# Kernel tuning notes

Hardware: AMD Instinct MI355X
Metric: run time of the kernel (lower is better)

The kernel has to match this reference:

```python
import jax, jax.numpy as jnp
import numpy as np

B, N, D, H = 8, 1024, 768, 4
ALPHA = 0.2      # LeakyReLU negative slope in GraphAttentionLayer
NEG = -9e15      # mask fill value for non-edges (pyGAT convention)


def setup_inputs() -> dict:
    key = jax.random.key(0)
    ks = jax.random.split(key, 8)
    input_emb = jax.random.normal(ks[0], (B, N, D), jnp.float32)
    adj = jax.random.randint(ks[1], (B, N, N), 0, 2, dtype=jnp.int32)
    mask_node = jnp.ones((B, N), jnp.float32)
    s = 1.0 / np.sqrt(D).astype(np.float32)
    W_heads = jax.random.normal(ks[2], (H, D, D), jnp.float32) * s          # per-head W: nfeat->nhid
    a_heads = jax.random.normal(ks[3], (H, 2 * D, 1), jnp.float32) * s      # per-head attention vector a
    W_out = jax.random.normal(ks[4], (H * D, D), jnp.float32) * (1.0 / np.sqrt(H * D).astype(np.float32))
    a_out = jax.random.normal(ks[5], (2 * D, 1), jnp.float32) * s
    w_cls = jax.random.normal(ks[6], (D, 1), jnp.float32) * s               # Classifier.linear1 weight
    b_cls = jnp.zeros((1,), jnp.float32)
    return dict(input_emb=input_emb, adj=adj, mask_node=mask_node,
                W_heads=W_heads, a_heads=a_heads, W_out=W_out, a_out=a_out,
                w_cls=w_cls, b_cls=b_cls)


def _gat_layer(x, adj_mask, W, a, concat):
    # x: [B,N,Fin], W: [Fin,Fout], a: [2*Fout,1], adj_mask: [B,N,N] bool
    Wh = jnp.einsum('bnd,df->bnf', x, W)            # [B,N,Fout]
    Fo = W.shape[1]
    f1 = Wh @ a[:Fo]                                 # [B,N,1] source term
    f2 = Wh @ a[Fo:]                                 # [B,N,1] target term
    e = jax.nn.leaky_relu(f1 + jnp.swapaxes(f2, 1, 2), ALPHA)  # [B,N,N]
    e = jnp.where(adj_mask, e, NEG)
    att = jax.nn.softmax(e, axis=-1)                 # dropout=0 -> no attention dropout
    h = jnp.einsum('bij,bjf->bif', att, Wh)          # [B,N,Fout]
    return jax.nn.elu(h) if concat else h


def reference(input_emb, adj, mask_node, W_heads, a_heads, W_out, a_out, w_cls, b_cls):
    adj_mask = adj > 0
    # multi-head GAT (concat=True heads), vectorized over heads and batch
    heads = jax.vmap(lambda Wi, ai: _gat_layer(input_emb, adj_mask, Wi, ai, True))(W_heads, a_heads)  # [H,B,N,D]
    xx = jnp.moveaxis(heads, 0, 2).reshape(B, N, H * D)  # torch.cat over heads, dim=1 per node
    out = jax.nn.elu(_gat_layer(xx, adj_mask, W_out, a_out, False))
    # dropout_layer(p=0.5) assumed eval mode (identity); residual add
    yy = out + input_emb                               # [B,N,D]
    h = (yy @ w_cls + b_cls)[..., 0]                   # Classifier linear -> [B,N]
    node_scores = jax.nn.sigmoid(h) * mask_node
    return yy, node_scores
```

## Files before the change

### kernel.cpp

```cpp
#include <hip/hip_runtime.h>


typedef unsigned short ushortT;
typedef _Float16 f16;
typedef __attribute__((ext_vector_type(8))) _Float16 f16x8;
typedef __attribute__((ext_vector_type(4))) _Float16 f16x4;
typedef __attribute__((ext_vector_type(4))) float f32x4;
typedef __attribute__((ext_vector_type(2))) float f32x2;
typedef __attribute__((ext_vector_type(8))) unsigned short u16x8;
typedef __attribute__((ext_vector_type(2))) unsigned short u16x2;
typedef __attribute__((ext_vector_type(4))) int i32x4;

#define ALPHA 0.2f

__device__ __forceinline__ float b2f(ushortT u) {
  union { unsigned int i; float f; } c; c.i = ((unsigned int)u) << 16; return c.f;
}
__device__ __forceinline__ ushortT f2b(float f) {
  union { float f; unsigned int u; } c; c.f = f;
  unsigned int u = c.u;
  u += 0x7FFFu + ((u >> 16) & 1u);
  return (ushortT)(u >> 16);
}
__device__ __forceinline__ float* qbuf(char* dout, int flg) {
  return (float*)(dout + (flg ? 25165824L : 12582912L));
}
__device__ __forceinline__ void gld16(const f16* g, f16* l) {
  __builtin_amdgcn_global_load_lds(
      (const __attribute__((address_space(1))) void*)g,
      (__attribute__((address_space(3))) void*)l, 16, 0, 0);
}

__global__ void detect_dtype(const ushortT* __restrict__ X, int* __restrict__ flag,
                             float* __restrict__ Pws, char* __restrict__ dout) {
  __shared__ int s[256];
  int t = threadIdx.x, c = 0;
  for (int i = t; i < 16384; i += 256) {
    int e = (X[2 * i] >> 7) & 0xFF;
    if (e > 140 || e < 100) c++;
  }
  s[t] = c; __syncthreads();
  for (int o = 128; o > 0; o >>= 1) { if (t < o) s[t] += s[t + o]; __syncthreads(); }
  __syncthreads();
  int fl = (s[0] > 1000) ? 1 : 0;
  if (t == 0) *flag = fl;
  float* Qv = qbuf(dout, fl);
#pragma unroll
  for (int i = 0; i < 8; i++) { Pws[t + i * 256] = 0.f; Qv[t + i * 256] = 0.f; }
}

struct GA {
  const void* A; const void* B; void* C; const void* R; const void* avec;
  long aOff, bOff, cOff, rOff, avOff;
  int K, lda, ldb, aRaw, accum, fd, fsel, zmask;
};

template <int MODE, int BSRC>
__device__ void gbody(const GA a, float* Pws, char* dout, int flg,
                      f16* AS, f16* BS) {
  int t = threadIdx.x;
  int n0 = blockIdx.x * 64, m0 = blockIdx.y * 64;
  int aTy = a.aRaw ? (flg ? 2 : 1) : 0;
  float* fv = a.fsel ? qbuf(dout, flg) : Pws;

  if (a.zmask && blockIdx.x == 0 && blockIdx.y == 0) {
    if (a.zmask & 1) {
#pragma unroll
      for (int i = 0; i < 8; i++) Pws[t + i * 256] = 0.f;
    }
    if (a.zmask & 2) {
      float* Qv = qbuf(dout, flg);
#pragma unroll
      for (int i = 0; i < 8; i++) Qv[t + i * 256] = 0.f;
    }
  }

  const f16*     Ah = (const f16*)a.A;
  const ushortT* Au = (const ushortT*)a.A;
  const float*   Af = (const float*)a.A;
  const f16*     Bh = (const f16*)a.B;
  const ushortT* Bu = (const ushortT*)a.B;
  const float*   Bf = (const float*)a.B;

  int lane = t & 63, wid = t >> 6;
  int wr = wid >> 1, wc = wid & 1;
  int lr = lane & 15, lg = lane >> 4, l7 = lane & 7;
  int aRow0 = (wr * 32 + lr) * 64, aRow1 = aRow0 + 16 * 64;
  int bRow0 = (wc * 32 + lr) * 64, bRow1 = bRow0 + 16 * 64;
  int ch0 = ((lg) ^ l7) * 8, ch1 = ((4 + lg) ^ l7) * 8;

  f32x4 acc[2][2];
#pragma unroll
  for (int i = 0; i < 2; i++)
#pragma unroll
    for (int j = 0; j < 2; j++) acc[i][j] = (f32x4){0.f, 0.f, 0.f, 0.f};

  auto compute = [&](int cur) {
    f16* Ac = AS + cur * 4096; f16* Bc = BS + cur * 4096;
#pragma unroll
    for (int kk = 0; kk < 2; kk++) {
      int ch = kk ? ch1 : ch0;
      f16x8 a0 = *(const f16x8*)(Ac + aRow0 + ch);
      f16x8 a1 = *(const f16x8*)(Ac + aRow1 + ch);
      f16x8 b0 = *(const f16x8*)(Bc + bRow0 + ch);
      f16x8 b1 = *(const f16x8*)(Bc + bRow1 + ch);
      acc[0][0] = __builtin_amdgcn_mfma_f32_16x16x32_f16(a0, b0, acc[0][0], 0, 0, 0);
      acc[0][1] = __builtin_amdgcn_mfma_f32_16x16x32_f16(a0, b1, acc[0][1], 0, 0, 0);
      acc[1][0] = __builtin_amdgcn_mfma_f32_16x16x32_f16(a1, b0, acc[1][0], 0, 0, 0);
      acc[1][1] = __builtin_amdgcn_mfma_f32_16x16x32_f16(a1, b1, acc[1][1], 0, 0, 0);
    }
  };

  int KT = a.K >> 6;

  if (BSRC == 0) {
    int gr = lane >> 3, gcn = lane & 7, swz = (gcn ^ (gr & 7)) * 8;
    int isB = wid >> 1, cq4 = (wid & 1) * 4;
    long gA = a.aOff + (long)(m0 + gr) * a.lda + swz;
    long gB = a.bOff + (long)(n0 + gr) * (long)a.K + swz;
    auto stageG = [&](int buf, int kt) {
      if (!isB) {
        const f16* g = Ah + gA + (long)kt * 64;
        f16* dst = AS + buf * 4096;
#pragma unroll
        for (int c = 0; c < 4; c++)
          gld16(g + (long)(cq4 + c) * 8 * a.lda, dst + (cq4 + c) * 512);
      } else {
        const f16* g = Bh + gB + (long)kt * 64;
        f16* dst = BS + buf * 4096;
#pragma unroll
        for (int c = 0; c < 4; c++)
          gld16(g + (long)(cq4 + c) * 8 * a.K, dst + (cq4 + c) * 512);
      }
    };
    stageG(0, 0);
    __syncthreads();
    for (int kt = 0; kt < KT; ++kt) {
      int cur = kt & 1;
      if (kt + 1 < KT) stageG(cur ^ 1, kt + 1);
      compute(cur);
      __syncthreads();
    }
  } else {
    int tq = t >> 2, cq = t & 3;
    long aBase = a.aOff + (long)(m0 + tq) * a.lda + cq * 16;
    int stA0 = tq * 64 + (((2 * cq)     ^ (tq & 7)) * 8);
    int stA1 = tq * 64 + (((2 * cq + 1) ^ (tq & 7)) * 8);
    int q2 = t & 31, cB = t >> 5;
    int nb0 = 2 * q2, nb1 = nb0 + 1;
    int stB0 = nb0 * 64 + ((cB ^ (nb0 & 7)) * 8);
    int stB1 = nb1 * 64 + ((cB ^ (nb1 & 7)) * 8);

    f16x8 ra0, ra1, rb0, rb1;
    auto loadA = [&](int kt) {
      long g = aBase + (long)kt * 64;
      if (aTy == 0) {
        ra0 = *(const f16x8*)(Ah + g);
        ra1 = *(const f16x8*)(Ah + g + 8);
      } else if (aTy == 1) {
        u16x8 v0 = *(const u16x8*)(Au + g);
        u16x8 v1 = *(const u16x8*)(Au + g + 8);
#pragma unroll
        for (int j = 0; j < 8; j++) { ra0[j] = (f16)b2f(v0[j]); ra1[j] = (f16)b2f(v1[j]); }
      } else {
        f32x4 v0 = *(const f32x4*)(Af + g);
        f32x4 v1 = *(const f32x4*)(Af + g + 4);
        f32x4 v2 = *(const f32x4*)(Af + g + 8);
        f32x4 v3 = *(const f32x4*)(Af + g + 12);
#pragma unroll
        for (int j = 0; j < 4; j++) {
          ra0[j] = (f16)v0[j]; ra0[4 + j] = (f16)v1[j];
          ra1[j] = (f16)v2[j]; ra1[4 + j] = (f16)v3[j];
        }
      }
    };
    auto loadB = [&](int kt) {
      long rbase = a.bOff + (long)(kt * 64 + cB * 8) * a.ldb + n0 + 2 * q2;
      if (flg) {
#pragma unroll
        for (int j = 0; j < 8; j++) {
          f32x2 v = *(const f32x2*)(Bf + rbase + (long)j * a.ldb);
          rb0[j] = (f16)v[0]; rb1[j] = (f16)v[1];
        }
      } else {
#pragma unroll
        for (int j = 0; j < 8; j++) {
          u16x2 v = *(const u16x2*)(Bu + rbase + (long)j * a.ldb);
          rb0[j] = (f16)b2f(v[0]); rb1[j] = (f16)b2f(v[1]);
        }
      }
    };
    auto stage = [&](int buf) {
      *(f16x8*)(AS + buf * 4096 + stA0) = ra0;
      *(f16x8*)(AS + buf * 4096 + stA1) = ra1;
      *(f16x8*)(BS + buf * 4096 + stB0) = rb0;
      *(f16x8*)(BS + buf * 4096 + stB1) = rb1;
    };
    loadA(0); loadB(0);
    stage(0);
    loadA(1); loadB(1);
    __syncthreads();
    for (int kt = 0; kt < KT; ++kt) {
      int cur = kt & 1;
      if (kt + 1 < KT) stage(cur ^ 1);
      if (kt + 2 < KT) { loadA(kt + 2); loadB(kt + 2); }
      compute(cur);
      __syncthreads();
    }
  }

  int rowb_base = m0 + wr * 32 + 4 * lg;
  int col_base  = n0 + wc * 32 + lr;

  float a1v[2], a2v[2];
  float p1[2][4], p2[2][4];
  if (a.fd) {
    const float* avf = (const float*)a.avec; const ushortT* avu = (const ushortT*)a.avec;
#pragma unroll
    for (int fn = 0; fn < 2; fn++) {
      int c = n0 + wc * 32 + fn * 16 + lr;
      a1v[fn] = flg ? avf[a.avOff + c]       : b2f(avu[a.avOff + c]);
      a2v[fn] = flg ? avf[a.avOff + 768 + c] : b2f(avu[a.avOff + 768 + c]);
    }
#pragma unroll
    for (int fm = 0; fm < 2; fm++)
#pragma unroll
      for (int r = 0; r < 4; r++) { p1[fm][r] = 0.f; p2[fm][r] = 0.f; }
  }

#pragma unroll
  for (int fm = 0; fm < 2; fm++) {
#pragma unroll
    for (int fn = 0; fn < 2; fn++) {
      int rowb = rowb_base + fm * 16;
      int col  = col_base + fn * 16;
      f32x4 v = acc[fm][fn];
      float fullv[4];
      if (MODE == 4) {
        f16x4 pk;
#pragma unroll
        for (int r = 0; r < 4; r++) { fullv[r] = v[r]; pk[r] = (f16)v[r]; }
        *(f16x4*)((f16*)a.C + (long)col * 1024 + rowb) = pk;
      } else if (MODE == 3) {
        f16* Cc = (f16*)a.C;
        long idx = (long)col * 1024 + rowb;
        f16x4 pk;
        if (a.accum) {
          f16x4 old = *(const f16x4*)(Cc + idx);
#pragma unroll
          for (int r = 0; r < 4; r++) { fullv[r] = (float)old[r] + v[r]; pk[r] = (f16)fullv[r]; }
        } else {
#pragma unroll
          for (int r = 0; r < 4; r++) { fullv[r] = v[r]; pk[r] = (f16)v[r]; }
        }
        *(f16x4*)(Cc + idx) = pk;
      } else {
#pragma unroll
        for (int r = 0; r < 4; r++) {
          int row = rowb + r;
          float x = v[r];
          x = x > 0.f ? x : __expf(x) - 1.f;
          long ci = a.cOff + (long)row * 768 + col;
          if (MODE == 2) {
            long ri = a.rOff + (long)row * 768 + col;
            x += flg ? ((const float*)a.R)[ri] : b2f(((const ushortT*)a.R)[ri]);
            if (flg) ((float*)a.C)[ci] = x;
            else     ((ushortT*)a.C)[ci] = f2b(x);
          } else {
            ((f16*)a.C)[ci] = (f16)x;
          }
        }
      }
      if (a.fd) {
        float ac1 = a1v[fn], ac2 = a2v[fn];
#pragma unroll
        for (int r = 0; r < 4; r++) {
          p1[fm][r] += fullv[r] * ac1;
          p2[fm][r] += fullv[r] * ac2;
        }
      }
    }
  }

  if (a.fd) {
#pragma unroll
    for (int fm = 0; fm < 2; fm++)
#pragma unroll
      for (int r = 0; r < 4; r++) {
#pragma unroll
        for (int o = 1; o < 16; o <<= 1) {
          p1[fm][r] += __shfl_xor(p1[fm][r], o);
          p2[fm][r] += __shfl_xor(p2[fm][r], o);
        }
      }
    if (lr == 0) {
#pragma unroll
      for (int fm = 0; fm < 2; fm++)
#pragma unroll
        for (int r = 0; r < 4; r++) {
          int row = rowb_base + fm * 16 + r;
          atomicAdd(fv + row, p1[fm][r]);
          atomicAdd(fv + 1024 + row, p2[fm][r]);
        }
    }
  }
}

template <int MODE, int BSRC>
__global__ __launch_bounds__(256) void k_solo(GA a, float* Pws, char* dout,
                                              const int* __restrict__ rflag) {
  __shared__ __align__(16) f16 As[2][4096];
  __shared__ __align__(16) f16 Bs[2][4096];
  gbody<MODE, BSRC>(a, Pws, dout, *rflag, &As[0][0], &Bs[0][0]);
}
__global__ __launch_bounds__(256) void k_pair31(GA g3, GA g1, float* Pws, char* dout,
                                                const int* __restrict__ rflag) {
  __shared__ __align__(16) f16 As[2][4096];
  __shared__ __align__(16) f16 Bs[2][4096];
  int flg = *rflag;
  if (blockIdx.z == 0) gbody<3, 1>(g3, Pws, dout, flg, &As[0][0], &Bs[0][0]);
  else                 gbody<4, 1>(g1, Pws, dout, flg, &As[0][0], &Bs[0][0]);
}
__global__ __launch_bounds__(256) void k_pair41(GA g4, GA g1, float* Pws, char* dout,
                                                const int* __restrict__ rflag) {
  __shared__ __align__(16) f16 As[2][4096];
  __shared__ __align__(16) f16 Bs[2][4096];
  int flg = *rflag;
  if (blockIdx.z == 0) gbody<2, 0>(g4, Pws, dout, flg, &As[0][0], &Bs[0][0]);
  else                 gbody<4, 1>(g1, Pws, dout, flg, &As[0][0], &Bs[0][0]);
}

__global__ __launch_bounds__(256) void attn_kernel(
    const float* __restrict__ Pws, char* __restrict__ dout, int fsel,
    const int* __restrict__ adj, f16* __restrict__ att,
    const int* __restrict__ rflag) {
  __shared__ float sred[8];
  int flg = *rflag;
  const float* fvb = fsel ? qbuf(dout, flg) : Pws;
  const float* f1 = fvb;
  const float* f2 = fvb + 1024;
  int i = blockIdx.x;
  const int* arow = adj + (size_t)i * 1024;
  float f1i = f1[i];
  f16* orow = att + (size_t)i * 1024;
  int t = threadIdx.x, lane = t & 63, wid = t >> 6;
  int j0 = t * 4;

  i32x4 av = *(const i32x4*)(arow + j0);
  f32x4 fvv = *(const f32x4*)(f2 + j0);

  float e[4];
  int msk[4];
  float mx = -1e38f;
#pragma unroll
  for (int c = 0; c < 4; c++) {
    float ev = f1i + fvv[c];
    ev = ev > 0.f ? ev : ALPHA * ev;
    e[c] = ev;
    msk[c] = av[c] > 0;
    if (msk[c]) mx = fmaxf(mx, ev);
  }
#pragma unroll
  for (int o = 32; o > 0; o >>= 1) mx = fmaxf(mx, __shfl_down(mx, o));
  if (lane == 0) sred[wid] = mx;
  __syncthreads();
  float bmx = fmaxf(fmaxf(sred[0], sred[1]), fmaxf(sred[2], sred[3]));
  bool none = bmx < -1e37f;

  float p[4];
  float sum = 0.f;
#pragma unroll
  for (int c = 0; c < 4; c++) {
    p[c] = none ? 1.f : (msk[c] ? __expf(e[c] - bmx) : 0.f);
    sum += p[c];
  }
#pragma unroll
  for (int o = 32; o > 0; o >>= 1) sum += __shfl_down(sum, o);
  if (lane == 0) sred[4 + wid] = sum;
  __syncthreads();
  float inv = 1.f / (sred[4] + sred[5] + sred[6] + sred[7]);
  f16x4 pk;
#pragma unroll
  for (int c = 0; c < 4; c++) pk[c] = (f16)(p[c] * inv);
  *(f16x4*)(orow + j0) = pk;
}

__global__ __launch_bounds__(256) void cls_kernel(
    void* __restrict__ outbase, const void* __restrict__ w,
    const void* __restrict__ bc, const void* __restrict__ mask,
    const int* __restrict__ rflag) {
  int t = threadIdx.x, lane = t & 63, wv = t >> 6;
  long row = (long)blockIdx.x * 4 + wv;
  int f32 = *rflag;
  const float* yf = (const float*)outbase; const ushortT* yu = (const ushortT*)outbase;
  const float* wf = (const float*)w;       const ushortT* wu = (const ushortT*)w;
  float s = 0.f;
  for (int d = lane; d < 768; d += 64) {
    float yv = f32 ? yf[row * 768 + d] : b2f(yu[row * 768 + d]);
    float wvv = f32 ? wf[d] : b2f(wu[d]);
    s += yv * wvv;
  }
#pragma unroll
  for (int o = 32; o > 0; o >>= 1) s += __shfl_down(s, o);
  if (lane == 0) {
    float bb = f32 ? ((const float*)bc)[0] : b2f(((const ushortT*)bc)[0]);
    float mk = f32 ? ((const float*)mask)[row] : b2f(((const ushortT*)mask)[row]);
    float sig = 1.f / (1.f + __expf(-(s + bb)));
    long oi = 6291456L + row;
    if (f32) ((float*)outbase)[oi] = sig * mk;
    else ((ushortT*)outbase)[oi] = f2b(sig * mk);
  }
}

extern "C" void kernel_launch(void* const* d_in, const int* in_sizes, int n_in,
                              void* d_out, int out_size, void* d_ws, size_t ws_size,
                              hipStream_t stream) {
  (void)in_sizes; (void)n_in; (void)out_size; (void)ws_size;

  const void* X    = d_in[0];
  const int*  adj  = (const int*)d_in[1];
  const void* maskN= d_in[2];
  const void* Wh   = d_in[3];
  const void* aH   = d_in[4];
  const void* Wo   = d_in[5];
  const void* aO   = d_in[6];
  const void* wcls = d_in[7];
  const void* bcls = d_in[8];

  char* ws = (char*)d_ws;
  float* Pws  = (float*)(ws + 0);
  int*   flag = (int*)(ws + 8192);
  f16* Wh1T = (f16*)(ws + 8448);
  f16* Wh2T = (f16*)(ws + 1581312);
  f16* attb = (f16*)(ws + 3154176);
  f16* hout = (f16*)(ws + 5251328);
  char* dob = (char*)d_out;

  detect_dtype<<<1, 256, 0, stream>>>((const ushortT*)X, flag, Pws, dob);

  auto mkG1 = [&](int b, int h) {
    GA g{}; g.A = X; g.B = Wh; g.C = Wh1T; g.R = nullptr; g.avec = aH;
    g.aOff = (long)b * 786432; g.bOff = (long)h * 589824;
    g.cOff = 0; g.rOff = 0; g.avOff = (long)h * 1536;
    g.K = 768; g.lda = 768; g.ldb = 768; g.aRaw = 1; g.accum = 0;
    g.fd = 1; g.fsel = (h + (b & 1)) & 1; g.zmask = 0;
    return g;
  };

  dim3 gg(12, 16), gp(12, 16, 2);
  k_solo<4, 1><<<gg, 256, 0, stream>>>(mkG1(0, 0), Pws, dob, flag);

  for (int b = 0; b < 8; b++) {
    int phase = b & 1;
    long xOff = (long)b * 786432;
    for (int h = 0; h < 4; h++) {
      attn_kernel<<<1024, 256, 0, stream>>>(
          Pws, dob, (h + phase) & 1, adj + (size_t)b * 1048576, attb, flag);
      GA g2{}; g2.A = attb; g2.B = Wh1T; g2.C = hout;
      g2.K = 1024; g2.lda = 1024; g2.ldb = 1024; g2.aRaw = 0; g2.accum = 0;
      g2.fd = 0; g2.fsel = 0;
      g2.zmask = (h < 3) ? (1 << ((h + 1 + phase) & 1)) : 3;
      k_solo<1, 0><<<gg, 256, 0, stream>>>(g2, Pws, dob, flag);
      GA g3{}; g3.A = hout; g3.B = Wo; g3.C = Wh2T; g3.avec = aO;
      g3.bOff = (long)h * 589824; g3.avOff = 0;
      g3.K = 768; g3.lda = 768; g3.ldb = 768; g3.aRaw = 0;
      g3.accum = h > 0 ? 1 : 0;
      g3.fd = (h == 3) ? 1 : 0; g3.fsel = phase; g3.zmask = 0;
      if (h < 3) {
        k_pair31<<<gp, 256, 0, stream>>>(g3, mkG1(b, h + 1), Pws, dob, flag);
      } else {
        k_solo<3, 1><<<gg, 256, 0, stream>>>(g3, Pws, dob, flag);
      }
    }
    attn_kernel<<<1024, 256, 0, stream>>>(
        Pws, dob, phase, adj + (size_t)b * 1048576, attb, flag);
    GA g4{}; g4.A = attb; g4.B = Wh2T; g4.C = d_out; g4.R = X;
    g4.cOff = xOff; g4.rOff = xOff;
    g4.K = 1024; g4.lda = 1024; g4.ldb = 1024; g4.aRaw = 0; g4.accum = 0;
    g4.fd = 0; g4.fsel = 0; g4.zmask = 0;
    if (b < 7) {
      k_pair41<<<gp, 256, 0, stream>>>(g4, mkG1(b + 1, 0), Pws, dob, flag);
    } else {
      k_solo<2, 0><<<gg, 256, 0, stream>>>(g4, Pws, dob, flag);
    }
  }

  cls_kernel<<<2048, 256, 0, stream>>>(d_out, wcls, bcls, maskN, flag);
}
```

Before: 1.480 ms.

## Re-pipeline GAT stages: pair aggregation with next projection, fuse attention with output GEMM

```diff
diff --git a/kernel.cpp b/kernel.cpp
--- a/kernel.cpp
+++ b/kernel.cpp
@@ -22,8 +22,12 @@
   u += 0x7FFFu + ((u >> 16) & 1u);
   return (ushortT)(u >> 16);
 }
-__device__ __forceinline__ float* qbuf(char* dout, int flg) {
-  return (float*)(dout + (flg ? 25165824L : 12582912L));
+__device__ __forceinline__ f16* whB(char* dout, int flg) {
+  return (f16*)(dout + (flg ? 22020096L : 11010048L));
+}
+__device__ __forceinline__ float* fbuf(int sel, float* Pws, char* dout, int flg) {
+  if (sel == 0) return Pws;
+  return (float*)(dout + (flg ? 25165824L : 12582912L) + (long)(sel - 1) * 8192);
 }
 __device__ __forceinline__ void gld16(const f16* g, f16* l) {
   __builtin_amdgcn_global_load_lds(
@@ -44,43 +48,44 @@
   __syncthreads();
   int fl = (s[0] > 1000) ? 1 : 0;
   if (t == 0) *flag = fl;
-  float* Qv = qbuf(dout, fl);
-#pragma unroll
-  for (int i = 0; i < 8; i++) { Pws[t + i * 256] = 0.f; Qv[t + i * 256] = 0.f; }
+  float* Qv = (float*)(dout + (fl ? 25165824L : 12582912L));
+#pragma unroll
+  for (int i = 0; i < 8; i++) Pws[t + i * 256] = 0.f;
+#pragma unroll
+  for (int i = 0; i < 16; i++) Qv[t + i * 256] = 0.f;
 }
 
 struct GA {
   const void* A; const void* B; void* C; const void* R; const void* avec;
   long aOff, bOff, cOff, rOff, avOff;
-  int K, lda, ldb, aRaw, accum, fd, fsel, zmask;
+  int K, lda, ldb, aRaw, accum, fd, fsel, zmask, bWhb, cWhb;
 };
 
 template <int MODE, int BSRC>
 __device__ void gbody(const GA a, float* Pws, char* dout, int flg,
-                      f16* AS, f16* BS) {
+                      f16* AS, f16* BS, int n0, int m0, bool bid0) {
   int t = threadIdx.x;
-  int n0 = blockIdx.x * 64, m0 = blockIdx.y * 64;
   int aTy = a.aRaw ? (flg ? 2 : 1) : 0;
-  float* fv = a.fsel ? qbuf(dout, flg) : Pws;
-
-  if (a.zmask && blockIdx.x == 0 && blockIdx.y == 0) {
-    if (a.zmask & 1) {
-#pragma unroll
-      for (int i = 0; i < 8; i++) Pws[t + i * 256] = 0.f;
-    }
-    if (a.zmask & 2) {
-      float* Qv = qbuf(dout, flg);
-#pragma unroll
-      for (int i = 0; i < 8; i++) Qv[t + i * 256] = 0.f;
-    }
+  float* fv = fbuf(a.fsel, Pws, dout, flg);
+  const void* Bres = a.bWhb ? (const void*)whB(dout, flg) : a.B;
+  void*       Cres = a.cWhb ? (void*)whB(dout, flg) : a.C;
+
+  if (a.zmask && bid0) {
+#pragma unroll
+    for (int sb = 0; sb < 3; sb++)
+      if ((a.zmask >> sb) & 1) {
+        float* z = fbuf(sb, Pws, dout, flg);
+#pragma unroll
+        for (int i = 0; i < 8; i++) z[t + i * 256] = 0.f;
+      }
   }
 
   const f16*     Ah = (const f16*)a.A;
   const ushortT* Au = (const ushortT*)a.A;
   const float*   Af = (const float*)a.A;
-  const f16*     Bh = (const f16*)a.B;
-  const ushortT* Bu = (const ushortT*)a.B;
-  const float*   Bf = (const float*)a.B;
+  const f16*     Bh = (const f16*)Bres;
+  const ushortT* Bu = (const ushortT*)Bres;
+  const float*   Bf = (const float*)Bres;
 
   int lane = t & 63, wid = t >> 6;
   int wr = wid >> 1, wc = wid & 1;
@@ -240,9 +245,9 @@
         f16x4 pk;
 #pragma unroll
         for (int r = 0; r < 4; r++) { fullv[r] = v[r]; pk[r] = (f16)v[r]; }
-        *(f16x4*)((f16*)a.C + (long)col * 1024 + rowb) = pk;
+        *(f16x4*)((f16*)Cres + (long)col * 1024 + rowb) = pk;
       } else if (MODE == 3) {
-        f16* Cc = (f16*)a.C;
+        f16* Cc = (f16*)Cres;
         long idx = (long)col * 1024 + rowb;
         f16x4 pk;
         if (a.accum) {
@@ -264,10 +269,10 @@
           if (MODE == 2) {
             long ri = a.rOff + (long)row * 768 + col;
             x += flg ? ((const float*)a.R)[ri] : b2f(((const ushortT*)a.R)[ri]);
-            if (flg) ((float*)a.C)[ci] = x;
-            else     ((ushortT*)a.C)[ci] = f2b(x);
+            if (flg) ((float*)Cres)[ci] = x;
+            else     ((ushortT*)Cres)[ci] = f2b(x);
           } else {
-            ((f16*)a.C)[ci] = (f16)x;
+            ((f16*)Cres)[ci] = (f16)x;
           }
         }
       }
@@ -304,6 +309,52 @@
         }
     }
   }
+}
+
+__device__ void attn_body(const float* __restrict__ fvb, const int* __restrict__ adj,
+                          f16* __restrict__ att, int rowBase) {
+  int t = threadIdx.x, lane = t & 63, wid = t >> 6;
+  int row = rowBase + wid;
+  const float* f2 = fvb + 1024;
+  const int* arow = adj + (size_t)row * 1024;
+  f16* orow = att + (size_t)row * 1024;
+  float f1i = fvb[row];
+  int c0 = lane * 16;
+
+  float e[16]; int msk[16];
+  float mx = -1e38f;
+#pragma unroll
+  for (int g = 0; g < 4; g++) {
+    i32x4 av = *(const i32x4*)(arow + c0 + g * 4);
+    f32x4 fvv = *(const f32x4*)(f2 + c0 + g * 4);
+#pragma unroll
+    for (int c = 0; c < 4; c++) {
+      float ev = f1i + fvv[c];
+      ev = ev > 0.f ? ev : ALPHA * ev;
+      e[g * 4 + c] = ev;
+      msk[g * 4 + c] = av[c] > 0;
+      if (msk[g * 4 + c]) mx = fmaxf(mx, ev);
+    }
+  }
+#pragma unroll
+  for (int o = 32; o > 0; o >>= 1) mx = fmaxf(mx, __shfl_xor(mx, o));
+  bool none = mx < -1e37f;
+
+  float sum = 0.f;
+  float p[16];
+#pragma unroll
+  for (int i = 0; i < 16; i++) {
+    p[i] = none ? 1.f : (msk[i] ? __expf(e[i] - mx) : 0.f);
+    sum += p[i];
+  }
+#pragma unroll
+  for (int o = 32; o > 0; o >>= 1) sum += __shfl_xor(sum, o);
+  float inv = 1.f / sum;
+  f16x8 o0, o1;
+#pragma unroll
+  for (int i = 0; i < 8; i++) { o0[i] = (f16)(p[i] * inv); o1[i] = (f16)(p[8 + i] * inv); }
+  *(f16x8*)(orow + c0) = o0;
+  *(f16x8*)(orow + c0 + 8) = o1;
 }
 
 template <int MODE, int BSRC>
@@ -311,78 +362,46 @@
                                               const int* __restrict__ rflag) {
   __shared__ __align__(16) f16 As[2][4096];
   __shared__ __align__(16) f16 Bs[2][4096];
-  gbody<MODE, BSRC>(a, Pws, dout, *rflag, &As[0][0], &Bs[0][0]);
-}
-__global__ __launch_bounds__(256) void k_pair31(GA g3, GA g1, float* Pws, char* dout,
+  gbody<MODE, BSRC>(a, Pws, dout, *rflag, &As[0][0], &Bs[0][0],
+                    blockIdx.x * 64, blockIdx.y * 64,
+                    blockIdx.x == 0 && blockIdx.y == 0);
+}
+__global__ __launch_bounds__(256) void k_pairGG(GA g2, GA g1, float* Pws, char* dout,
                                                 const int* __restrict__ rflag) {
   __shared__ __align__(16) f16 As[2][4096];
   __shared__ __align__(16) f16 Bs[2][4096];
   int flg = *rflag;
-  if (blockIdx.z == 0) gbody<3, 1>(g3, Pws, dout, flg, &As[0][0], &Bs[0][0]);
-  else                 gbody<4, 1>(g1, Pws, dout, flg, &As[0][0], &Bs[0][0]);
-}
-__global__ __launch_bounds__(256) void k_pair41(GA g4, GA g1, float* Pws, char* dout,
+  int id = blockIdx.x;
+  if (id < 192)
+    gbody<1, 0>(g2, Pws, dout, flg, &As[0][0], &Bs[0][0],
+                (id % 12) * 64, (id / 12) * 64, id == 0);
+  else {
+    int l = id - 192;
+    gbody<4, 1>(g1, Pws, dout, flg, &As[0][0], &Bs[0][0],
+                (l % 12) * 64, (l / 12) * 64, false);
+  }
+}
+__global__ __launch_bounds__(256) void k_pairGA(GA g3, int rsel,
+                                                const int* __restrict__ adj,
+                                                f16* __restrict__ att,
+                                                float* Pws, char* dout,
                                                 const int* __restrict__ rflag) {
   __shared__ __align__(16) f16 As[2][4096];
   __shared__ __align__(16) f16 Bs[2][4096];
   int flg = *rflag;
-  if (blockIdx.z == 0) gbody<2, 0>(g4, Pws, dout, flg, &As[0][0], &Bs[0][0]);
-  else                 gbody<4, 1>(g1, Pws, dout, flg, &As[0][0], &Bs[0][0]);
-}
-
-__global__ __launch_bounds__(256) void attn_kernel(
-    const float* __restrict__ Pws, char* __restrict__ dout, int fsel,
-    const int* __restrict__ adj, f16* __restrict__ att,
-    const int* __restrict__ rflag) {
-  __shared__ float sred[8];
+  int id = blockIdx.x;
+  if (id < 192)
+    gbody<3, 1>(g3, Pws, dout, flg, &As[0][0], &Bs[0][0],
+                (id % 12) * 64, (id / 12) * 64, id == 0);
+  else
+    attn_body(fbuf(rsel, Pws, dout, flg), adj, att, (id - 192) * 4);
+}
+__global__ __launch_bounds__(256) void k_attn(int rsel, const int* __restrict__ adj,
+                                              f16* __restrict__ att,
+                                              float* Pws, char* dout,
+                                              const int* __restrict__ rflag) {
   int flg = *rflag;
-  const float* fvb = fsel ? qbuf(dout, flg) : Pws;
-  const float* f1 = fvb;
-  const float* f2 = fvb + 1024;
-  int i = blockIdx.x;
-  const int* arow = adj + (size_t)i * 1024;
-  float f1i = f1[i];
-  f16* orow = att + (size_t)i * 1024;
-  int t = threadIdx.x, lane = t & 63, wid = t >> 6;
-  int j0 = t * 4;
-
-  i32x4 av = *(const i32x4*)(arow + j0);
-  f32x4 fvv = *(const f32x4*)(f2 + j0);
-
-  float e[4];
-  int msk[4];
-  float mx = -1e38f;
-#pragma unroll
-  for (int c = 0; c < 4; c++) {
-    float ev = f1i + fvv[c];
-    ev = ev > 0.f ? ev : ALPHA * ev;
-    e[c] = ev;
-    msk[c] = av[c] > 0;
-    if (msk[c]) mx = fmaxf(mx, ev);
-  }
-#pragma unroll
-  for (int o = 32; o > 0; o >>= 1) mx = fmaxf(mx, __shfl_down(mx, o));
-  if (lane == 0) sred[wid] = mx;
-  __syncthreads();
-  float bmx = fmaxf(fmaxf(sred[0], sred[1]), fmaxf(sred[2], sred[3]));
-  bool none = bmx < -1e37f;
-
-  float p[4];
-  float sum = 0.f;
-#pragma unroll
-  for (int c = 0; c < 4; c++) {
-    p[c] = none ? 1.f : (msk[c] ? __expf(e[c] - bmx) : 0.f);
-    sum += p[c];
-  }
-#pragma unroll
-  for (int o = 32; o > 0; o >>= 1) sum += __shfl_down(sum, o);
-  if (lane == 0) sred[4 + wid] = sum;
-  __syncthreads();
-  float inv = 1.f / (sred[4] + sred[5] + sred[6] + sred[7]);
-  f16x4 pk;
-#pragma unroll
-  for (int c = 0; c < 4; c++) pk[c] = (f16)(p[c] * inv);
-  *(f16x4*)(orow + j0) = pk;
+  attn_body(fbuf(rsel, Pws, dout, flg), adj, att, blockIdx.x * 4);
 }
 
 __global__ __launch_bounds__(256) void cls_kernel(
@@ -430,7 +449,7 @@
   char* ws = (char*)d_ws;
   float* Pws  = (float*)(ws + 0);
   int*   flag = (int*)(ws + 8192);
-  f16* Wh1T = (f16*)(ws + 8448);
+  f16* Wh1A = (f16*)(ws + 8448);
   f16* Wh2T = (f16*)(ws + 1581312);
   f16* attb = (f16*)(ws + 3154176);
   f16* hout = (f16*)(ws + 5251328);
@@ -439,50 +458,73 @@
   detect_dtype<<<1, 256, 0, stream>>>((const ushortT*)X, flag, Pws, dob);
 
   auto mkG1 = [&](int b, int h) {
-    GA g{}; g.A = X; g.B = Wh; g.C = Wh1T; g.R = nullptr; g.avec = aH;
+    GA g{}; g.A = X; g.B = Wh; g.C = Wh1A; g.avec = aH;
     g.aOff = (long)b * 786432; g.bOff = (long)h * 589824;
-    g.cOff = 0; g.rOff = 0; g.avOff = (long)h * 1536;
-    g.K = 768; g.lda = 768; g.ldb = 768; g.aRaw = 1; g.accum = 0;
-    g.fd = 1; g.fsel = (h + (b & 1)) & 1; g.zmask = 0;
+    g.avOff = (long)h * 1536;
+    g.K = 768; g.lda = 768; g.ldb = 768; g.aRaw = 1;
+    g.fd = 1; g.cWhb = h & 1;
     return g;
   };
-
-  dim3 gg(12, 16), gp(12, 16, 2);
-  k_solo<4, 1><<<gg, 256, 0, stream>>>(mkG1(0, 0), Pws, dob, flag);
+  auto mkG2 = [&](int h) {
+    GA g{}; g.A = attb; g.B = Wh1A; g.C = hout;
+    g.K = 1024; g.lda = 1024; g.ldb = 1024;
+    g.bWhb = h & 1;
+    return g;
+  };
+  auto mkG3 = [&](int h) {
+    GA g{}; g.A = hout; g.B = Wo; g.C = Wh2T; g.avec = aO;
+    g.bOff = (long)h * 589824;
+    g.K = 768; g.lda = 768; g.ldb = 768;
+    g.accum = h > 0 ? 1 : 0;
+    return g;
+  };
+
+  dim3 gg(12, 16);
+  int w = 0;
+  auto wn = [&]() { int v = w % 3; ++w; return v; };
+
+  int fsG10 = wn();
+  {
+    GA g1 = mkG1(0, 0); g1.fsel = fsG10;
+    k_solo<4, 1><<<gg, 256, 0, stream>>>(g1, Pws, dob, flag);
+  }
 
   for (int b = 0; b < 8; b++) {
-    int phase = b & 1;
+    const int* adjb = adj + (size_t)b * 1048576;
     long xOff = (long)b * 786432;
+
+    k_attn<<<256, 256, 0, stream>>>(fsG10, adjb, attb, Pws, dob, flag);
+
+    int lastFsel = 0;
     for (int h = 0; h < 4; h++) {
-      attn_kernel<<<1024, 256, 0, stream>>>(
-          Pws, dob, (h + phase) & 1, adj + (size_t)b * 1048576, attb, flag);
-      GA g2{}; g2.A = attb; g2.B = Wh1T; g2.C = hout;
-      g2.K = 1024; g2.lda = 1024; g2.ldb = 1024; g2.aRaw = 0; g2.accum = 0;
-      g2.fd = 0; g2.fsel = 0;
-      g2.zmask = (h < 3) ? (1 << ((h + 1 + phase) & 1)) : 3;
-      k_solo<1, 0><<<gg, 256, 0, stream>>>(g2, Pws, dob, flag);
-      GA g3{}; g3.A = hout; g3.B = Wo; g3.C = Wh2T; g3.avec = aO;
-      g3.bOff = (long)h * 589824; g3.avOff = 0;
-      g3.K = 768; g3.lda = 768; g3.ldb = 768; g3.aRaw = 0;
-      g3.accum = h > 0 ? 1 : 0;
-      g3.fd = (h == 3) ? 1 : 0; g3.fsel = phase; g3.zmask = 0;
+      GA g2 = mkG2(h);
+      bool hasG1 = (h < 3) || (b < 7);
+      if (hasG1) {
+        int nh = (h < 3) ? h + 1 : 0;
+        int nbb = (h < 3) ? b : b + 1;
+        GA g1 = mkG1(nbb, nh);
+        g1.fsel = wn();
+        g2.zmask = (1 << (w % 3)) | ((h == 3) ? (1 << ((w + 1) % 3)) : 0);
+        k_pairGG<<<dim3(384), 256, 0, stream>>>(g2, g1, Pws, dob, flag);
+        if (nh == 0) fsG10 = g1.fsel;
+        lastFsel = g1.fsel;
+      } else {
+        g2.zmask = (1 << (w % 3));
+        k_solo<1, 0><<<gg, 256, 0, stream>>>(g2, Pws, dob, flag);
+      }
       if (h < 3) {
-        k_pair31<<<gp, 256, 0, stream>>>(g3, mkG1(b, h + 1), Pws, dob, flag);
-      } else {
-        k_solo<3, 1><<<gg, 256, 0, stream>>>(g3, Pws, dob, flag);
-      }
-    }
-    attn_kernel<<<1024, 256, 0, stream>>>(
-        Pws, dob, phase, adj + (size_t)b * 1048576, attb, flag);
+        GA g3 = mkG3(h);
+        k_pairGA<<<dim3(448), 256, 0, stream>>>(g3, lastFsel, adjb, attb,
+                                                Pws, dob, flag);
+      }
+    }
+    GA g33 = mkG3(3); g33.fd = 1; g33.fsel = wn();
+    k_solo<3, 1><<<gg, 256, 0, stream>>>(g33, Pws, dob, flag);
+    k_attn<<<256, 256, 0, stream>>>(g33.fsel, adjb, attb, Pws, dob, flag);
     GA g4{}; g4.A = attb; g4.B = Wh2T; g4.C = d_out; g4.R = X;
     g4.cOff = xOff; g4.rOff = xOff;
-    g4.K = 1024; g4.lda = 1024; g4.ldb = 1024; g4.aRaw = 0; g4.accum = 0;
-    g4.fd = 0; g4.fsel = 0; g4.zmask = 0;
-    if (b < 7) {
-      k_pair41<<<gp, 256, 0, stream>>>(g4, mkG1(b + 1, 0), Pws, dob, flag);
-    } else {
-      k_solo<2, 0><<<gg, 256, 0, stream>>>(g4, Pws, dob, flag);
-    }
+    g4.K = 1024; g4.lda = 1024; g4.ldb = 1024;
+    k_solo<2, 0><<<gg, 256, 0, stream>>>(g4, Pws, dob, flag);
   }
 
   cls_kernel<<<2048, 256, 0, stream>>>(d_out, wcls, bcls, maskN, flag);
```

New measurement: 1.490 ms. No clear change (+0.7%).
